# Performance work log

Hardware: AMD Instinct MI355X
Metric: run time of the kernel (lower is better)

The kernel has to match this reference:

```python
import jax, jax.numpy as jnp
import numpy as np

POOL_SIZE = 7


def setup_inputs() -> dict:
    key = jax.random.key(0)
    k1, k2, k3 = jax.random.split(key, 3)
    B, H, W, C = 1, 128, 128, 1024
    N = 512
    shared_layers = jax.random.normal(k1, (B, H, W, C), dtype=jnp.float32)
    # Build valid boxes [ymin, xmin, ymax, xmax] with min <= max, inside the map.
    mins = jax.random.uniform(k2, (N, 2), minval=0.0, maxval=float(H - 2))
    spans = jax.random.uniform(k3, (N, 2), minval=1.0, maxval=32.0)
    maxs = jnp.minimum(mins + spans, float(H - 1))
    rois = jnp.stack([mins[:, 0], mins[:, 1], maxs[:, 0], maxs[:, 1]], axis=1).astype(jnp.float32)
    return {"shared_layers": shared_layers, "rois": rois}


def reference(shared_layers, rois):
    """Per-ROI crop + bilinear resize (TF1 resize_bilinear, align_corners=False),
    concatenated over ROIs then flattened. Fully vectorized over ROIs."""
    P = POOL_SIZE
    B, H, W, C = shared_layers.shape  # B == 1 as in the original usage
    feat = shared_layers[0]  # [H, W, C]

    ymin = rois[:, 0].astype(jnp.int32)
    xmin = rois[:, 1].astype(jnp.int32)
    ymax = rois[:, 2].astype(jnp.int32)
    xmax = rois[:, 3].astype(jnp.int32)
    h = (ymax - ymin + 1).astype(jnp.float32)  # [N]
    w = (xmax - xmin + 1).astype(jnp.float32)

    grid = jnp.arange(P, dtype=jnp.float32)  # [P]
    # TF resize_bilinear (align_corners=False): src = out_idx * in_size / out_size
    src_y = grid[None, :] * (h[:, None] / P)  # [N, P]
    src_x = grid[None, :] * (w[:, None] / P)  # [N, P]

    y0 = jnp.floor(src_y).astype(jnp.int32)
    x0 = jnp.floor(src_x).astype(jnp.int32)
    y1 = jnp.minimum(y0 + 1, (ymax - ymin)[:, None])
    x1 = jnp.minimum(x0 + 1, (xmax - xmin)[:, None])
    fy = (src_y - y0.astype(jnp.float32))[:, :, None, None]  # [N, P, 1, 1]
    fx = (src_x - x0.astype(jnp.float32))[:, None, :, None]  # [N, 1, P, 1]

    gy0 = ymin[:, None] + y0  # [N, P] global row indices
    gy1 = ymin[:, None] + y1
    gx0 = xmin[:, None] + x0  # [N, P] global col indices
    gx1 = xmin[:, None] + x1

    # 4 corner gathers -> [N, P, P, C]
    tl = feat[gy0[:, :, None], gx0[:, None, :]]
    tr = feat[gy0[:, :, None], gx1[:, None, :]]
    bl = feat[gy1[:, :, None], gx0[:, None, :]]
    br = feat[gy1[:, :, None], gx1[:, None, :]]

    top = tl + (tr - tl) * fx
    bot = bl + (br - bl) * fx
    out = top + (bot - top) * fy  # [N, P, P, C]

    return out.reshape(out.shape[0], -1)  # Flatten -> [N, P*P*C]
```

## Files before the change

kernel.cpp:

```cpp
#include <hip/hip_runtime.h>


#define POOL_P 7
#define FEAT_C 1024
#define FEAT_W 128
#define CELLS_PER_ROI (POOL_P * POOL_P)
#define GROUP_BLOCKS  (8 * CELLS_PER_ROI)

__global__ __launch_bounds__(128) void roi_pool_kernel(
    const float* __restrict__ feat,
    const float* __restrict__ rois,
    float* __restrict__ out)
{
    const int i    = blockIdx.x;
    const int q    = i / GROUP_BLOCKS;
    const int k    = i - q * GROUP_BLOCKS;
    const int r    = 8 * q + (k & 7);
    const int cell = k >> 3;
    const int px   = cell % POOL_P;
    const int py   = cell / POOL_P;

    const float4 roi = ((const float4*)rois)[r];
    const int ymin = (int)roi.x;
    const int xmin = (int)roi.y;
    const int ymax = (int)roi.z;
    const int xmax = (int)roi.w;

    const float h = (float)(ymax - ymin + 1);
    const float w = (float)(xmax - xmin + 1);

    const float src_y = (float)py * (h / 7.0f);
    const float src_x = (float)px * (w / 7.0f);

    const int y0 = (int)floorf(src_y);
    const int x0 = (int)floorf(src_x);
    const int y1 = min(y0 + 1, ymax - ymin);
    const int x1 = min(x0 + 1, xmax - xmin);

    const float fy = src_y - (float)y0;
    const float fx = src_x - (float)x0;

    const int gy0 = ymin + y0;
    const int gy1 = ymin + y1;
    const int gx0 = xmin + x0;
    const int gx1 = xmin + x1;

    const float4* __restrict__ tlp = (const float4*)(feat + ((size_t)(gy0 * FEAT_W + gx0)) * FEAT_C);
    const float4* __restrict__ trp = (const float4*)(feat + ((size_t)(gy0 * FEAT_W + gx1)) * FEAT_C);
    const float4* __restrict__ blp = (const float4*)(feat + ((size_t)(gy1 * FEAT_W + gx0)) * FEAT_C);
    const float4* __restrict__ brp = (const float4*)(feat + ((size_t)(gy1 * FEAT_W + gx1)) * FEAT_C);
    float4* __restrict__ op = (float4*)(out + ((size_t)r * CELLS_PER_ROI + cell) * FEAT_C);

    const int t0 = threadIdx.x;
    const int t1 = t0 + 128;

    const float4 tl0 = tlp[t0];
    const float4 tr0 = trp[t0];
    const float4 bl0 = blp[t0];
    const float4 br0 = brp[t0];
    const float4 tl1 = tlp[t1];
    const float4 tr1 = trp[t1];
    const float4 bl1 = blp[t1];
    const float4 br1 = brp[t1];

    float4 res0, res1;
    {
        float top, bot;
        top = tl0.x + (tr0.x - tl0.x) * fx; bot = bl0.x + (br0.x - bl0.x) * fx; res0.x = top + (bot - top) * fy;
        top = tl0.y + (tr0.y - tl0.y) * fx; bot = bl0.y + (br0.y - bl0.y) * fx; res0.y = top + (bot - top) * fy;
        top = tl0.z + (tr0.z - tl0.z) * fx; bot = bl0.z + (br0.z - bl0.z) * fx; res0.z = top + (bot - top) * fy;
        top = tl0.w + (tr0.w - tl0.w) * fx; bot = bl0.w + (br0.w - bl0.w) * fx; res0.w = top + (bot - top) * fy;
        top = tl1.x + (tr1.x - tl1.x) * fx; bot = bl1.x + (br1.x - bl1.x) * fx; res1.x = top + (bot - top) * fy;
        top = tl1.y + (tr1.y - tl1.y) * fx; bot = bl1.y + (br1.y - bl1.y) * fx; res1.y = top + (bot - top) * fy;
        top = tl1.z + (tr1.z - tl1.z) * fx; bot = bl1.z + (br1.z - bl1.z) * fx; res1.z = top + (bot - top) * fy;
        top = tl1.w + (tr1.w - tl1.w) * fx; bot = bl1.w + (br1.w - bl1.w) * fx; res1.w = top + (bot - top) * fy;
    }
    op[t0] = res0;
    op[t1] = res1;
}

extern "C" void kernel_launch(void* const* d_in, const int* in_sizes, int n_in,
                              void* d_out, int out_size, void* d_ws, size_t ws_size,
                              hipStream_t stream) {
    const float* feat = (const float*)d_in[0];
    const float* rois = (const float*)d_in[1];
    float* out        = (float*)d_out;

    const int n_rois   = in_sizes[1] / 4;
    const int n_blocks = n_rois * CELLS_PER_ROI;

    roi_pool_kernel<<<n_blocks, 128, 0, stream>>>(feat, rois, out);
}
```

Before: 170.2 us.

## Process full output row per block, reuse corner columns, skip zero-weight loads

Each block now computes one output row (seven cells) of an ROI with 256 threads, so each thread covers one float4 of the channel vector. Corner columns shared between adjacent cells are kept in registers instead of being reloaded. Loads for neighbours with zero interpolation weight or a clamped index are skipped. Outputs are written with nontemporal stores to avoid polluting the cache. This cuts redundant global reads of the feature map, at the cost of serial per-block work, fewer blocks, and some branching.

```diff
diff --git a/kernel.cpp b/kernel.cpp
--- a/kernel.cpp
+++ b/kernel.cpp
@@ -4,21 +4,20 @@
 #define POOL_P 7
 #define FEAT_C 1024
 #define FEAT_W 128
-#define CELLS_PER_ROI (POOL_P * POOL_P)
-#define GROUP_BLOCKS  (8 * CELLS_PER_ROI)
+#define GROUP_BLOCKS (8 * POOL_P)
 
-__global__ __launch_bounds__(128) void roi_pool_kernel(
+typedef float vfloat4 __attribute__((ext_vector_type(4)));
+
+__global__ __launch_bounds__(256) void roi_pool_kernel(
     const float* __restrict__ feat,
     const float* __restrict__ rois,
     float* __restrict__ out)
 {
-    const int i    = blockIdx.x;
-    const int q    = i / GROUP_BLOCKS;
-    const int k    = i - q * GROUP_BLOCKS;
-    const int r    = 8 * q + (k & 7);
-    const int cell = k >> 3;
-    const int px   = cell % POOL_P;
-    const int py   = cell / POOL_P;
+    const int i  = blockIdx.x;
+    const int q  = i / GROUP_BLOCKS;
+    const int k  = i - q * GROUP_BLOCKS;
+    const int r  = 8 * q + (k & 7);
+    const int py = k >> 3;
 
     const float4 roi = ((const float4*)rois)[r];
     const int ymin = (int)roi.x;
@@ -30,53 +29,83 @@
     const float w = (float)(xmax - xmin + 1);
 
     const float src_y = (float)py * (h / 7.0f);
-    const float src_x = (float)px * (w / 7.0f);
+    const int y0 = (int)floorf(src_y);
+    const int y1 = min(y0 + 1, ymax - ymin);
+    const float fy = src_y - (float)y0;
+    const bool ny = (y1 != y0) && (fy != 0.0f);
 
-    const int y0 = (int)floorf(src_y);
-    const int x0 = (int)floorf(src_x);
-    const int y1 = min(y0 + 1, ymax - ymin);
-    const int x1 = min(x0 + 1, xmax - xmin);
+    const float* __restrict__ row0 = feat + (size_t)((ymin + y0) * FEAT_W) * FEAT_C;
+    const float* __restrict__ row1 = feat + (size_t)((ymin + y1) * FEAT_W) * FEAT_C;
 
-    const float fy = src_y - (float)y0;
-    const float fx = src_x - (float)x0;
+    const int t = threadIdx.x;
 
-    const int gy0 = ymin + y0;
-    const int gy1 = ymin + y1;
-    const int gx0 = xmin + x0;
-    const int gx1 = xmin + x1;
+    vfloat4* __restrict__ op = (vfloat4*)(out + ((size_t)r * 49 + (size_t)py * 7) * FEAT_C);
 
-    const float4* __restrict__ tlp = (const float4*)(feat + ((size_t)(gy0 * FEAT_W + gx0)) * FEAT_C);
-    const float4* __restrict__ trp = (const float4*)(feat + ((size_t)(gy0 * FEAT_W + gx1)) * FEAT_C);
-    const float4* __restrict__ blp = (const float4*)(feat + ((size_t)(gy1 * FEAT_W + gx0)) * FEAT_C);
-    const float4* __restrict__ brp = (const float4*)(feat + ((size_t)(gy1 * FEAT_W + gx1)) * FEAT_C);
-    float4* __restrict__ op = (float4*)(out + ((size_t)r * CELLS_PER_ROI + cell) * FEAT_C);
+    int X0[POOL_P], X1[POOL_P];
+    float FX[POOL_P];
+    const float wstep = w / 7.0f;
+    #pragma unroll
+    for (int px = 0; px < POOL_P; ++px) {
+        const float sx = (float)px * wstep;
+        const int x0 = (int)floorf(sx);
+        X0[px] = x0;
+        X1[px] = min(x0 + 1, xmax - xmin);
+        FX[px] = sx - (float)x0;
+    }
 
-    const int t0 = threadIdx.x;
-    const int t1 = t0 + 128;
+    float4 tl, tr, bl, br;
+    int colA = -1, colB = -1;
 
-    const float4 tl0 = tlp[t0];
-    const float4 tr0 = trp[t0];
-    const float4 bl0 = blp[t0];
-    const float4 br0 = brp[t0];
-    const float4 tl1 = tlp[t1];
-    const float4 tr1 = trp[t1];
-    const float4 bl1 = blp[t1];
-    const float4 br1 = brp[t1];
+    #pragma unroll
+    for (int px = 0; px < POOL_P; ++px) {
+        const int cL = X0[px];
+        const int cR = X1[px];
+        const bool needR = (cR != cL) && (FX[px] != 0.0f);
 
-    float4 res0, res1;
-    {
-        float top, bot;
-        top = tl0.x + (tr0.x - tl0.x) * fx; bot = bl0.x + (br0.x - bl0.x) * fx; res0.x = top + (bot - top) * fy;
-        top = tl0.y + (tr0.y - tl0.y) * fx; bot = bl0.y + (br0.y - bl0.y) * fx; res0.y = top + (bot - top) * fy;
-        top = tl0.z + (tr0.z - tl0.z) * fx; bot = bl0.z + (br0.z - bl0.z) * fx; res0.z = top + (bot - top) * fy;
-        top = tl0.w + (tr0.w - tl0.w) * fx; bot = bl0.w + (br0.w - bl0.w) * fx; res0.w = top + (bot - top) * fy;
-        top = tl1.x + (tr1.x - tl1.x) * fx; bot = bl1.x + (br1.x - bl1.x) * fx; res1.x = top + (bot - top) * fy;
-        top = tl1.y + (tr1.y - tl1.y) * fx; bot = bl1.y + (br1.y - bl1.y) * fx; res1.y = top + (bot - top) * fy;
-        top = tl1.z + (tr1.z - tl1.z) * fx; bot = bl1.z + (br1.z - bl1.z) * fx; res1.z = top + (bot - top) * fy;
-        top = tl1.w + (tr1.w - tl1.w) * fx; bot = bl1.w + (br1.w - bl1.w) * fx; res1.w = top + (bot - top) * fy;
+        float4 ntl, ntr, nbl, nbr;
+
+        if (cL == colA)      { ntl = tl; nbl = bl; }
+        else if (cL == colB) { ntl = tr; nbl = br; }
+        else {
+            const float* p0 = row0 + (size_t)(xmin + cL) * FEAT_C;
+            ntl = ((const float4*)p0)[t];
+            if (ny) {
+                const float* p1 = row1 + (size_t)(xmin + cL) * FEAT_C;
+                nbl = ((const float4*)p1)[t];
+            } else nbl = ntl;
+        }
+
+        if (!needR)          { ntr = ntl; nbr = nbl; }
+        else if (cR == colB) { ntr = tr; nbr = br; }
+        else {
+            const float* p0 = row0 + (size_t)(xmin + cR) * FEAT_C;
+            ntr = ((const float4*)p0)[t];
+            if (ny) {
+                const float* p1 = row1 + (size_t)(xmin + cR) * FEAT_C;
+                nbr = ((const float4*)p1)[t];
+            } else nbr = ntr;
+        }
+
+        tl = ntl; tr = ntr; bl = nbl; br = nbr;
+        colA = cL;
+        colB = needR ? cR : cL;
+
+        const float fxv = FX[px];
+        vfloat4 res;
+        {
+            float top;
+            top = tl.x + (tr.x - tl.x) * fxv;
+            res.x = ny ? top + ((bl.x + (br.x - bl.x) * fxv) - top) * fy : top;
+            top = tl.y + (tr.y - tl.y) * fxv;
+            res.y = ny ? top + ((bl.y + (br.y - bl.y) * fxv) - top) * fy : top;
+            top = tl.z + (tr.z - tl.z) * fxv;
+            res.z = ny ? top + ((bl.z + (br.z - bl.z) * fxv) - top) * fy : top;
+            top = tl.w + (tr.w - tl.w) * fxv;
+            res.w = ny ? top + ((bl.w + (br.w - bl.w) * fxv) - top) * fy : top;
+        }
+
+        __builtin_nontemporal_store(res, &op[(size_t)px * 256 + t]);
     }
-    op[t0] = res0;
-    op[t1] = res1;
 }
 
 extern "C" void kernel_launch(void* const* d_in, const int* in_sizes, int n_in,
@@ -87,7 +116,7 @@
     float* out        = (float*)d_out;
 
     const int n_rois   = in_sizes[1] / 4;
-    const int n_blocks = n_rois * CELLS_PER_ROI;
+    const int n_blocks = n_rois * POOL_P;
 
-    roi_pool_kernel<<<n_blocks, 128, 0, stream>>>(feat, rois, out);
+    roi_pool_kernel<<<n_blocks, 256, 0, stream>>>(feat, rois, out);
 }
```

Result: slower. 173.9 us (+2.2%).
